# Kernel tuning notes

Hardware: AMD Instinct MI355X
Metric: run time of the kernel (lower is better)

## Reference

```python
import jax, jax.numpy as jnp
import numpy as np

B, N_AIM, N_DET, C = 4, 2048, 2048, 256  # inplanes=256, inter_channels=128


def _lin(x, w, b):
    # torch nn.Linear: y = x @ W^T + b, weight shape [out, in]
    return jnp.einsum('bnc,dc->bnd', x, w) + b


def setup_inputs() -> dict:
    key = jax.random.key(0)
    ks = jax.random.split(key, 16)
    s = 1.0 / np.sqrt(C)
    inp = {
        'detect': jax.random.normal(ks[0], (B, N_DET, C), jnp.float32),
        'aim': jax.random.normal(ks[1], (B, N_AIM, C), jnp.float32),
    }
    names = ['g', 'g2', 'theta', 'phi', 'W', 'Q']
    for i, nm in enumerate(names):
        inp[nm + '_w'] = jax.random.uniform(ks[2 + 2 * i], (C, C), jnp.float32, -s, s)
        inp[nm + '_b'] = jax.random.uniform(ks[3 + 2 * i], (C,), jnp.float32, -s, s)
    return inp


def reference(detect, aim, g_w, g_b, g2_w, g2_b, theta_w, theta_b, phi_w, phi_b, W_w, W_b, Q_w, Q_b):
    b, na, c = aim.shape
    nd = detect.shape[1]
    ic = c // 2  # inter_channels

    # view(B, ic, -1) on a contiguous [B, N, C] tensor -> row-major reshape to [B, ic, 2N]
    d_x = _lin(detect, g_w, g_b).reshape(b, ic, -1).transpose(0, 2, 1)      # (B, 2Nd, ic)
    a_x = _lin(aim, g2_w, g2_b).reshape(b, ic, -1).transpose(0, 2, 1)       # (B, 2Na, ic)
    theta_x = _lin(aim, theta_w, theta_b).reshape(b, ic, -1).transpose(0, 2, 1)  # (B, 2Na, ic)
    phi_x = _lin(detect, phi_w, phi_b).reshape(b, ic, -1)                   # (B, ic, 2Nd)

    f = jnp.matmul(theta_x, phi_x)                 # (B, 2Na, 2Nd)
    f_div_C = f / f.shape[-1]                      # scale by 2*Nd
    fi_div_C = jnp.swapaxes(f, 1, 2) / f.shape[-2] # (B, 2Nd, 2Na), scale by 2*Na

    non_aim = jnp.matmul(f_div_C, d_x)             # (B, 2Na, ic)
    non_aim = non_aim.transpose(0, 2, 1).reshape(b, na, c)
    non_aim = _lin(non_aim, W_w, W_b) + aim

    non_det = jnp.matmul(fi_div_C, a_x)            # (B, 2Nd, ic)
    non_det = non_det.transpose(0, 2, 1).reshape(b, nd, c)
    non_det = _lin(non_det, Q_w, Q_b) + detect

    return (non_det, non_aim)
```

## Files before the change

### kernel.cpp

```cpp
#include <hip/hip_runtime.h>


typedef __attribute__((ext_vector_type(4))) float  f32x4;
typedef __attribute__((ext_vector_type(8))) __bf16 bf16x8;
typedef __attribute__((ext_vector_type(8))) unsigned short u16x8;
typedef __attribute__((ext_vector_type(4))) unsigned short u16x4;

__device__ inline unsigned short f2bf(float f) {
    union { float f; unsigned u; } c; c.f = f;
    unsigned r = c.u + 0x7FFF + ((c.u >> 16) & 1);
    return (unsigned short)(r >> 16);
}
__device__ inline bf16x8 ldfrag(const unsigned short* p) {
    return __builtin_bit_cast(bf16x8, *(const u16x8*)p);
}

__global__ __launch_bounds__(256)
void prep_kernel(const float* __restrict__ g_w, const float* __restrict__ g2_w,
                 const float* __restrict__ th_w, const float* __restrict__ ph_w,
                 const float* __restrict__ W_w, const float* __restrict__ Q_w,
                 const float* __restrict__ aim, const float* __restrict__ detect,
                 unsigned short* __restrict__ dst)
{
    const int z = blockIdx.y;
    const float* src; size_t n4; unsigned short* o;
    if (z == 0)      { src = g_w;    n4 = 16384;  o = dst; }
    else if (z == 1) { src = g2_w;   n4 = 16384;  o = dst + 65536; }
    else if (z == 2) { src = th_w;   n4 = 16384;  o = dst + 2 * 65536; }
    else if (z == 3) { src = ph_w;   n4 = 16384;  o = dst + 3 * 65536; }
    else if (z == 4) { src = W_w;    n4 = 16384;  o = dst + 4 * 65536; }
    else if (z == 5) { src = Q_w;    n4 = 16384;  o = dst + 5 * 65536; }
    else if (z == 6) { src = aim;    n4 = 524288; o = dst + 6 * 65536; }
    else             { src = detect; n4 = 524288; o = dst + 6 * 65536 + 2097152; }
    const size_t stride = (size_t)gridDim.x * 256;
    for (size_t i = blockIdx.x * 256 + threadIdx.x; i < n4; i += stride) {
        float4 v = ((const float4*)src)[i];
        u16x4 p; p[0]=f2bf(v.x); p[1]=f2bf(v.y); p[2]=f2bf(v.z); p[3]=f2bf(v.w);
        ((u16x4*)o)[i] = p;
    }
}

__global__ __launch_bounds__(256)
void lin4_kernel(const unsigned short* __restrict__ Abf, const unsigned short* __restrict__ Dbf,
                 const unsigned short* __restrict__ Wb,
                 const float* __restrict__ b_g, const float* __restrict__ b_g2,
                 const float* __restrict__ b_th, const float* __restrict__ b_ph,
                 unsigned short* __restrict__ T,  unsigned short* __restrict__ Ga,
                 unsigned short* __restrict__ P,  unsigned short* __restrict__ Gd)
{
    const int z = blockIdx.z, set = blockIdx.x;
    const unsigned short* A = z ? Dbf : Abf;
    const int wslot = z ? (set ? 0 : 3) : (set ? 1 : 2);
    const unsigned short* Wm = Wb + (size_t)wslot * 65536;
    const float* Bv = z ? (set ? b_g : b_ph) : (set ? b_g2 : b_th);
    unsigned short* O = z ? (set ? Gd : P) : (set ? Ga : T);
    const int m0 = blockIdx.y * 64;

    __shared__ unsigned short As[64][40];
    __shared__ unsigned short Bs[256][40];

    const int tid = threadIdx.x, lane = tid & 63, w = tid >> 6;
    const int wr = w >> 1, wc = w & 1, q = lane >> 4, ln = lane & 15;

    f32x4 acc[2][8] = {};

    for (int k0 = 0; k0 < 256; k0 += 32) {
        {
            int row = tid >> 2, c8 = tid & 3;
            *(u16x8*)&As[row][c8 * 8] = *(const u16x8*)(A + (size_t)(m0 + row) * 256 + k0 + c8 * 8);
        }
        #pragma unroll
        for (int i = 0; i < 4; ++i) {
            int c = tid + i * 256, row = c >> 2, c8 = c & 3;
            *(u16x8*)&Bs[row][c8 * 8] = *(const u16x8*)(Wm + (size_t)row * 256 + k0 + c8 * 8);
        }
        __syncthreads();
        bf16x8 af[2], bb[8];
        #pragma unroll
        for (int i = 0; i < 2; ++i) af[i] = ldfrag(&As[wr * 32 + i * 16 + ln][q * 8]);
        #pragma unroll
        for (int j = 0; j < 8; ++j) bb[j] = ldfrag(&Bs[wc * 128 + j * 16 + ln][q * 8]);
        #pragma unroll
        for (int i = 0; i < 2; ++i)
            #pragma unroll
            for (int j = 0; j < 8; ++j)
                acc[i][j] = __builtin_amdgcn_mfma_f32_16x16x32_bf16(af[i], bb[j], acc[i][j], 0, 0, 0);
        __syncthreads();
    }

    #pragma unroll
    for (int i = 0; i < 2; ++i)
        #pragma unroll
        for (int j = 0; j < 8; ++j) {
            int n = wc * 128 + j * 16 + ln;
            float bias = Bv[n];
            #pragma unroll
            for (int r = 0; r < 4; ++r) {
                int m = m0 + wr * 32 + i * 16 + q * 4 + r;
                O[(size_t)m * 256 + n] = f2bf(acc[i][j][r] + bias);
            }
        }
}

__global__ __launch_bounds__(256)
void mid_kernel(const unsigned short* __restrict__ Gd, const unsigned short* __restrict__ P,
                const unsigned short* __restrict__ Ga, const unsigned short* __restrict__ T,
                const unsigned short* __restrict__ Wb,
                float* __restrict__ Spart,
                unsigned short* __restrict__ TW, unsigned short* __restrict__ PQ)
{
    __shared__ unsigned short lds[13824];

    const int tid = threadIdx.x, lane = tid & 63, w = tid >> 6;
    const int wr = w >> 1, wc = w & 1, q = lane >> 4, ln = lane & 15;

    if (blockIdx.x < 256) {
        const int bz = blockIdx.x;
        const int which = bz >> 7, rem = bz & 127, batch = rem >> 5;
        const int mhalf = (rem >> 4) & 1, chunk = rem & 15;
        const unsigned short* A = (which ? Ga : Gd) + (size_t)batch * 524288;
        const unsigned short* B = (which ? T  : P ) + (size_t)batch * 524288;
        float* out = Spart + ((size_t)(which * 4 + batch) * 16 + chunk) * 16384;
        const int kbeg = chunk * 256, m0 = mhalf * 64;

        unsigned short (*As)[72] = (unsigned short (*)[72])lds;
        unsigned short (*Bs)[72] = (unsigned short (*)[72])(lds + 64 * 72);

        f32x4 acc[2][4] = {};

        for (int kk = 0; kk < 4; ++kk) {
            const int k0 = kbeg + kk * 64;
            #pragma unroll
            for (int i = 0; i < 2; ++i) {
                int c = tid + i * 256, row = c >> 3, c8 = c & 7;
                *(u16x8*)&As[row][c8 * 8] = *(const u16x8*)(A + (size_t)(m0 + row) * 4096 + k0 + c8 * 8);
            }
            #pragma unroll
            for (int i = 0; i < 4; ++i) {
                int c = tid + i * 256, row = c >> 3, c8 = c & 7;
                *(u16x8*)&Bs[row][c8 * 8] = *(const u16x8*)(B + (size_t)row * 4096 + k0 + c8 * 8);
            }
            __syncthreads();
            #pragma unroll
            for (int ks = 0; ks < 2; ++ks) {
                bf16x8 af[2], bb[4];
                #pragma unroll
                for (int i = 0; i < 2; ++i) af[i] = ldfrag(&As[wr * 32 + i * 16 + ln][ks * 32 + q * 8]);
                #pragma unroll
                for (int j = 0; j < 4; ++j) bb[j] = ldfrag(&Bs[wc * 64 + j * 16 + ln][ks * 32 + q * 8]);
                #pragma unroll
                for (int i = 0; i < 2; ++i)
                    #pragma unroll
                    for (int j = 0; j < 4; ++j)
                        acc[i][j] = __builtin_amdgcn_mfma_f32_16x16x32_bf16(af[i], bb[j], acc[i][j], 0, 0, 0);
            }
            __syncthreads();
        }

        #pragma unroll
        for (int i = 0; i < 2; ++i)
            #pragma unroll
            for (int j = 0; j < 4; ++j)
                #pragma unroll
                for (int r = 0; r < 4; ++r) {
                    int m = m0 + wr * 32 + i * 16 + q * 4 + r, n = wc * 64 + j * 16 + ln;
                    out[m * 128 + n] = acc[i][j][r];
                }
    } else {
        const int t = blockIdx.x - 256;
        const int side = t >> 8, rem = t & 255, mtile = rem >> 1, nhalf = rem & 1;
        const unsigned short* A = side ? P : T;
        const unsigned short* Wm = Wb + (size_t)(4 + side) * 65536;
        unsigned short* O = side ? PQ : TW;
        const int m0 = mtile * 64, n0 = nhalf * 128;

        unsigned short (*As)[40] = (unsigned short (*)[40])lds;
        unsigned short (*Bs)[40] = (unsigned short (*)[40])(lds + 64 * 40);

        f32x4 acc[2][4] = {};

        for (int k0 = 0; k0 < 256; k0 += 32) {
            {
                int row = tid >> 2, c8 = tid & 3;
                *(u16x8*)&As[row][c8 * 8] = *(const u16x8*)(A + (size_t)(m0 + row) * 256 + k0 + c8 * 8);
            }
            #pragma unroll
            for (int i = 0; i < 2; ++i) {
                int c = tid + i * 256, row = c >> 2, c8 = c & 3;
                *(u16x8*)&Bs[row][c8 * 8] = *(const u16x8*)(Wm + (size_t)(n0 + row) * 256 + k0 + c8 * 8);
            }
            __syncthreads();
            bf16x8 af[2], bb[4];
            #pragma unroll
            for (int i = 0; i < 2; ++i) af[i] = ldfrag(&As[wr * 32 + i * 16 + ln][q * 8]);
            #pragma unroll
            for (int j = 0; j < 4; ++j) bb[j] = ldfrag(&Bs[wc * 64 + j * 16 + ln][q * 8]);
            #pragma unroll
            for (int i = 0; i < 2; ++i)
                #pragma unroll
                for (int j = 0; j < 4; ++j)
                    acc[i][j] = __builtin_amdgcn_mfma_f32_16x16x32_bf16(af[i], bb[j], acc[i][j], 0, 0, 0);
            __syncthreads();
        }

        #pragma unroll
        for (int i = 0; i < 2; ++i)
            #pragma unroll
            for (int j = 0; j < 4; ++j) {
                int n = n0 + wc * 64 + j * 16 + ln;
                #pragma unroll
                for (int r = 0; r < 4; ++r) {
                    int m = m0 + wr * 32 + i * 16 + q * 4 + r;
                    O[(size_t)m * 256 + n] = f2bf(acc[i][j][r]);
                }
            }
    }
}

__global__ __launch_bounds__(256)
void sred_kernel(const float* __restrict__ Spart, unsigned short* __restrict__ Sbf)
{
    const int idx = blockIdx.x * 256 + threadIdx.x;
    const int c = idx >> 14, e = idx & 16383;
    float s = 0.f;
    #pragma unroll
    for (int k = 0; k < 16; ++k) s += Spart[((size_t)(c * 16 + k) << 14) + e];
    Sbf[idx] = f2bf(s * (1.0f / 4096.0f));
}

__global__ __launch_bounds__(256)
void combine_kernel(const unsigned short* __restrict__ Sbf,
                    const unsigned short* __restrict__ TW, const unsigned short* __restrict__ PQ,
                    const float* __restrict__ W_b, const float* __restrict__ Q_b,
                    const float* __restrict__ aim, const float* __restrict__ detect,
                    float* __restrict__ out_aim, float* __restrict__ out_det)
{
    const int which = blockIdx.z >> 2, batch = blockIdx.z & 3;
    const int qq = blockIdx.y;
    const int dtile = blockIdx.x >> 1, ihalf = blockIdx.x & 1;
    const int d0 = dtile * 128, i0 = ihalf * 64;
    const unsigned short* Sm = Sbf + (size_t)(which * 4 + batch) * 16384;
    const unsigned short* Bsrc = (which ? PQ : TW) + (size_t)batch * 524288;
    const float* Bv = which ? Q_b : W_b;
    const float* R  = (which ? detect : aim) + (size_t)batch * 524288;
    float* O = (which ? out_det : out_aim) + (size_t)batch * 524288;

    __shared__ unsigned short As[64][72];
    __shared__ unsigned short Bs[128][72];

    const int tid = threadIdx.x, lane = tid & 63, w = tid >> 6;
    const int wr = w >> 1, wc = w & 1, q = lane >> 4, ln = lane & 15;

    f32x4 acc[2][4] = {};

    for (int kk = 0; kk < 2; ++kk) {
        const int k0 = kk * 64;
        #pragma unroll
        for (int i = 0; i < 2; ++i) {
            int c = tid + i * 256, row = c >> 3, c8 = c & 7;
            *(u16x8*)&As[row][c8 * 8] = *(const u16x8*)(Sm + (size_t)(i0 + row) * 128 + k0 + c8 * 8);
        }
        #pragma unroll
        for (int i = 0; i < 4; ++i) {
            int c = tid + i * 256, krow = c >> 4, dc = (c & 15) * 8;
            int gr = 16 * (k0 + krow) + qq;
            u16x8 v = *(const u16x8*)(Bsrc + (size_t)gr * 256 + d0 + dc);
            #pragma unroll
            for (int jj = 0; jj < 8; ++jj) Bs[dc + jj][krow] = v[jj];
        }
        __syncthreads();
        #pragma unroll
        for (int ks = 0; ks < 2; ++ks) {
            bf16x8 af[2], bb[4];
            #pragma unroll
            for (int i = 0; i < 2; ++i) af[i] = ldfrag(&As[wr * 32 + i * 16 + ln][ks * 32 + q * 8]);
            #pragma unroll
            for (int j = 0; j < 4; ++j) bb[j] = ldfrag(&Bs[wc * 64 + j * 16 + ln][ks * 32 + q * 8]);
            #pragma unroll
            for (int i = 0; i < 2; ++i)
                #pragma unroll
                for (int j = 0; j < 4; ++j)
                    acc[i][j] = __builtin_amdgcn_mfma_f32_16x16x32_bf16(af[i], bb[j], acc[i][j], 0, 0, 0);
        }
        __syncthreads();
    }

    #pragma unroll
    for (int i = 0; i < 2; ++i)
        #pragma unroll
        for (int j = 0; j < 4; ++j) {
            int d = d0 + wc * 64 + j * 16 + ln;
            float bias = Bv[d];
            #pragma unroll
            for (int r = 0; r < 4; ++r) {
                int iS = i0 + wr * 32 + i * 16 + q * 4 + r;
                size_t off = (size_t)(16 * iS + qq) * 256 + d;
                O[off] = acc[i][j][r] + bias + R[off];
            }
        }
}

extern "C" void kernel_launch(void* const* d_in, const int* in_sizes, int n_in,
                              void* d_out, int out_size, void* d_ws, size_t ws_size,
                              hipStream_t stream)
{
    const float* detect = (const float*)d_in[0];
    const float* aim    = (const float*)d_in[1];
    const float* g_w  = (const float*)d_in[2];  const float* g_b  = (const float*)d_in[3];
    const float* g2_w = (const float*)d_in[4];  const float* g2_b = (const float*)d_in[5];
    const float* th_w = (const float*)d_in[6];  const float* th_b = (const float*)d_in[7];
    const float* ph_w = (const float*)d_in[8];  const float* ph_b = (const float*)d_in[9];
    const float* W_w  = (const float*)d_in[10]; const float* W_b  = (const float*)d_in[11];
    const float* Q_w  = (const float*)d_in[12]; const float* Q_b  = (const float*)d_in[13];

    const size_t TOT = 8192L * 256;

    unsigned short* ws16 = (unsigned short*)d_ws;
    unsigned short* Wbf = ws16;
    unsigned short* Abf = Wbf + 6 * 65536;
    unsigned short* Dbf = Abf + TOT;
    unsigned short* T   = Dbf + TOT;
    unsigned short* P   = T  + TOT;
    unsigned short* Gd  = P  + TOT;
    unsigned short* Ga  = Gd + TOT;
    unsigned short* TW  = Ga + TOT;
    unsigned short* PQ  = TW + TOT;
    unsigned short* Sbf = PQ + TOT;
    float* Spart = (float*)(Sbf + 131072);

    float* out_det = (float*)d_out;
    float* out_aim = out_det + TOT;

    prep_kernel<<<dim3(256, 8), 256, 0, stream>>>(
        g_w, g2_w, th_w, ph_w, W_w, Q_w, aim, detect, Wbf);
    lin4_kernel<<<dim3(2, 128, 2), 256, 0, stream>>>(
        Abf, Dbf, Wbf, g_b, g2_b, th_b, ph_b, T, Ga, P, Gd);
    mid_kernel<<<dim3(768), 256, 0, stream>>>(Gd, P, Ga, T, Wbf, Spart, TW, PQ);
    sred_kernel<<<dim3(512), 256, 0, stream>>>(Spart, Sbf);
    combine_kernel<<<dim3(4, 16, 8), 256, 0, stream>>>(
        Sbf, TW, PQ, W_b, Q_b, aim, detect, out_aim, out_det);
}
```

Before: 143.2 us.

## Fuse all five stages into one persistent kernel with grid barriers

Replaces the five separate launches (prep, linear projections, mid GEMMs, reduction, combine) with a single 512-block persistent kernel. The stages are separated by atomic-counter grid barriers that are reset by a memset each call. The f-matrix partial GEMM is re-tiled to 64x64 outputs so it fits into 512 blocks, and the W/Q projection is placed in the same barrier phase. The aim is to remove launch gaps and tail effects between kernels. In exchange it relies on all 512 blocks being co-resident, adds barrier spin overhead, and sets occupancy via launch_bounds(256,2).

```diff
diff --git a/kernel.cpp b/kernel.cpp
--- a/kernel.cpp
+++ b/kernel.cpp
@@ -15,130 +15,251 @@
     return __builtin_bit_cast(bf16x8, *(const u16x8*)p);
 }
 
-__global__ __launch_bounds__(256)
-void prep_kernel(const float* __restrict__ g_w, const float* __restrict__ g2_w,
-                 const float* __restrict__ th_w, const float* __restrict__ ph_w,
-                 const float* __restrict__ W_w, const float* __restrict__ Q_w,
-                 const float* __restrict__ aim, const float* __restrict__ detect,
-                 unsigned short* __restrict__ dst)
-{
-    const int z = blockIdx.y;
-    const float* src; size_t n4; unsigned short* o;
-    if (z == 0)      { src = g_w;    n4 = 16384;  o = dst; }
-    else if (z == 1) { src = g2_w;   n4 = 16384;  o = dst + 65536; }
-    else if (z == 2) { src = th_w;   n4 = 16384;  o = dst + 2 * 65536; }
-    else if (z == 3) { src = ph_w;   n4 = 16384;  o = dst + 3 * 65536; }
-    else if (z == 4) { src = W_w;    n4 = 16384;  o = dst + 4 * 65536; }
-    else if (z == 5) { src = Q_w;    n4 = 16384;  o = dst + 5 * 65536; }
-    else if (z == 6) { src = aim;    n4 = 524288; o = dst + 6 * 65536; }
-    else             { src = detect; n4 = 524288; o = dst + 6 * 65536 + 2097152; }
-    const size_t stride = (size_t)gridDim.x * 256;
-    for (size_t i = blockIdx.x * 256 + threadIdx.x; i < n4; i += stride) {
-        float4 v = ((const float4*)src)[i];
-        u16x4 p; p[0]=f2bf(v.x); p[1]=f2bf(v.y); p[2]=f2bf(v.z); p[3]=f2bf(v.w);
-        ((u16x4*)o)[i] = p;
-    }
-}
-
-__global__ __launch_bounds__(256)
-void lin4_kernel(const unsigned short* __restrict__ Abf, const unsigned short* __restrict__ Dbf,
-                 const unsigned short* __restrict__ Wb,
-                 const float* __restrict__ b_g, const float* __restrict__ b_g2,
-                 const float* __restrict__ b_th, const float* __restrict__ b_ph,
-                 unsigned short* __restrict__ T,  unsigned short* __restrict__ Ga,
-                 unsigned short* __restrict__ P,  unsigned short* __restrict__ Gd)
-{
-    const int z = blockIdx.z, set = blockIdx.x;
-    const unsigned short* A = z ? Dbf : Abf;
-    const int wslot = z ? (set ? 0 : 3) : (set ? 1 : 2);
-    const unsigned short* Wm = Wb + (size_t)wslot * 65536;
-    const float* Bv = z ? (set ? b_g : b_ph) : (set ? b_g2 : b_th);
-    unsigned short* O = z ? (set ? Gd : P) : (set ? Ga : T);
-    const int m0 = blockIdx.y * 64;
-
-    __shared__ unsigned short As[64][40];
-    __shared__ unsigned short Bs[256][40];
-
-    const int tid = threadIdx.x, lane = tid & 63, w = tid >> 6;
-    const int wr = w >> 1, wc = w & 1, q = lane >> 4, ln = lane & 15;
-
-    f32x4 acc[2][8] = {};
-
-    for (int k0 = 0; k0 < 256; k0 += 32) {
-        {
-            int row = tid >> 2, c8 = tid & 3;
-            *(u16x8*)&As[row][c8 * 8] = *(const u16x8*)(A + (size_t)(m0 + row) * 256 + k0 + c8 * 8);
-        }
-        #pragma unroll
-        for (int i = 0; i < 4; ++i) {
-            int c = tid + i * 256, row = c >> 2, c8 = c & 3;
-            *(u16x8*)&Bs[row][c8 * 8] = *(const u16x8*)(Wm + (size_t)row * 256 + k0 + c8 * 8);
-        }
-        __syncthreads();
-        bf16x8 af[2], bb[8];
-        #pragma unroll
-        for (int i = 0; i < 2; ++i) af[i] = ldfrag(&As[wr * 32 + i * 16 + ln][q * 8]);
-        #pragma unroll
-        for (int j = 0; j < 8; ++j) bb[j] = ldfrag(&Bs[wc * 128 + j * 16 + ln][q * 8]);
-        #pragma unroll
-        for (int i = 0; i < 2; ++i)
-            #pragma unroll
-            for (int j = 0; j < 8; ++j)
-                acc[i][j] = __builtin_amdgcn_mfma_f32_16x16x32_bf16(af[i], bb[j], acc[i][j], 0, 0, 0);
-        __syncthreads();
-    }
-
-    #pragma unroll
-    for (int i = 0; i < 2; ++i)
-        #pragma unroll
-        for (int j = 0; j < 8; ++j) {
-            int n = wc * 128 + j * 16 + ln;
-            float bias = Bv[n];
-            #pragma unroll
-            for (int r = 0; r < 4; ++r) {
-                int m = m0 + wr * 32 + i * 16 + q * 4 + r;
-                O[(size_t)m * 256 + n] = f2bf(acc[i][j][r] + bias);
-            }
-        }
-}
-
-__global__ __launch_bounds__(256)
-void mid_kernel(const unsigned short* __restrict__ Gd, const unsigned short* __restrict__ P,
-                const unsigned short* __restrict__ Ga, const unsigned short* __restrict__ T,
-                const unsigned short* __restrict__ Wb,
-                float* __restrict__ Spart,
-                unsigned short* __restrict__ TW, unsigned short* __restrict__ PQ)
+#define NBLK 512u
+
+__device__ inline void gridbar(unsigned* bar, int slot) {
+    __syncthreads();
+    if (threadIdx.x == 0) {
+        __threadfence();
+        __hip_atomic_fetch_add(bar + slot, 1u, __ATOMIC_RELAXED, __HIP_MEMORY_SCOPE_AGENT);
+        while (__hip_atomic_load(bar + slot, __ATOMIC_RELAXED, __HIP_MEMORY_SCOPE_AGENT) < NBLK)
+            __builtin_amdgcn_s_sleep(8);
+        __threadfence();
+    }
+    __syncthreads();
+}
+
+struct MegaArgs {
+    const float *detect, *aim;
+    const float *g_w, *g2_w, *th_w, *ph_w, *W_w, *Q_w;
+    const float *b_g, *b_g2, *b_th, *b_ph, *b_W, *b_Q;
+    unsigned short *Wbf, *Abf, *Dbf, *T, *P, *Gd, *Ga, *TW, *PQ, *Sbf;
+    float *Spart, *out_aim, *out_det;
+    unsigned *bar;
+};
+
+__global__ __launch_bounds__(256, 2)
+void mega_kernel(MegaArgs a)
 {
     __shared__ unsigned short lds[13824];
 
-    const int tid = threadIdx.x, lane = tid & 63, w = tid >> 6;
+    const int bid = blockIdx.x, tid = threadIdx.x;
+    const int lane = tid & 63, w = tid >> 6;
     const int wr = w >> 1, wc = w & 1, q = lane >> 4, ln = lane & 15;
 
-    if (blockIdx.x < 256) {
-        const int bz = blockIdx.x;
-        const int which = bz >> 7, rem = bz & 127, batch = rem >> 5;
-        const int mhalf = (rem >> 4) & 1, chunk = rem & 15;
-        const unsigned short* A = (which ? Ga : Gd) + (size_t)batch * 524288;
-        const unsigned short* B = (which ? T  : P ) + (size_t)batch * 524288;
-        float* out = Spart + ((size_t)(which * 4 + batch) * 16 + chunk) * 16384;
-        const int kbeg = chunk * 256, m0 = mhalf * 64;
+    if (bid < 44) {
+        for (int i = bid * 256 + tid; i < 98304; i += 44 * 256) {
+            int wsel = i >> 14, off = i & 16383;
+            const float* src = wsel == 0 ? a.g_w : wsel == 1 ? a.g2_w : wsel == 2 ? a.th_w :
+                               wsel == 3 ? a.ph_w : wsel == 4 ? a.W_w : a.Q_w;
+            float4 v = ((const float4*)src)[off];
+            u16x4 p; p[0]=f2bf(v.x); p[1]=f2bf(v.y); p[2]=f2bf(v.z); p[3]=f2bf(v.w);
+            ((u16x4*)(a.Wbf + (size_t)wsel * 65536))[off] = p;
+        }
+    } else {
+        const int r = bid - 44;
+        const float* src = r < 234 ? a.aim : a.detect;
+        unsigned short* o = r < 234 ? a.Abf : a.Dbf;
+        const int rb = r < 234 ? r : r - 234;
+        for (int i = rb * 256 + tid; i < 524288; i += 234 * 256) {
+            float4 v = ((const float4*)src)[i];
+            u16x4 p; p[0]=f2bf(v.x); p[1]=f2bf(v.y); p[2]=f2bf(v.z); p[3]=f2bf(v.w);
+            ((u16x4*)o)[i] = p;
+        }
+    }
+    gridbar(a.bar, 0);
+
+    {
+        const int z = bid >> 8, rem = bid & 255, set = rem & 1, mtile = rem >> 1;
+        const unsigned short* Ap = z ? a.Dbf : a.Abf;
+        const int wslot = z ? (set ? 0 : 3) : (set ? 1 : 2);
+        const unsigned short* Wm = a.Wbf + (size_t)wslot * 65536;
+        const float* Bv = z ? (set ? a.b_g : a.b_ph) : (set ? a.b_g2 : a.b_th);
+        unsigned short* O = z ? (set ? a.Gd : a.P) : (set ? a.Ga : a.T);
+        const int m0 = mtile * 64;
+
+        unsigned short (*As)[40] = (unsigned short (*)[40])lds;
+        unsigned short (*Bs)[40] = (unsigned short (*)[40])(lds + 64 * 40);
+
+        f32x4 acc[2][8] = {};
+
+        for (int k0 = 0; k0 < 256; k0 += 32) {
+            {
+                int row = tid >> 2, c8 = tid & 3;
+                *(u16x8*)&As[row][c8 * 8] = *(const u16x8*)(Ap + (size_t)(m0 + row) * 256 + k0 + c8 * 8);
+            }
+            #pragma unroll
+            for (int i = 0; i < 4; ++i) {
+                int c = tid + i * 256, row = c >> 2, c8 = c & 3;
+                *(u16x8*)&Bs[row][c8 * 8] = *(const u16x8*)(Wm + (size_t)row * 256 + k0 + c8 * 8);
+            }
+            __syncthreads();
+            bf16x8 af[2], bb[8];
+            #pragma unroll
+            for (int i = 0; i < 2; ++i) af[i] = ldfrag(&As[wr * 32 + i * 16 + ln][q * 8]);
+            #pragma unroll
+            for (int j = 0; j < 8; ++j) bb[j] = ldfrag(&Bs[wc * 128 + j * 16 + ln][q * 8]);
+            #pragma unroll
+            for (int i = 0; i < 2; ++i)
+                #pragma unroll
+                for (int j = 0; j < 8; ++j)
+                    acc[i][j] = __builtin_amdgcn_mfma_f32_16x16x32_bf16(af[i], bb[j], acc[i][j], 0, 0, 0);
+            __syncthreads();
+        }
+
+        #pragma unroll
+        for (int i = 0; i < 2; ++i)
+            #pragma unroll
+            for (int j = 0; j < 8; ++j) {
+                int n = wc * 128 + j * 16 + ln;
+                float bias = Bv[n];
+                #pragma unroll
+                for (int r = 0; r < 4; ++r) {
+                    int m = m0 + wr * 32 + i * 16 + q * 4 + r;
+                    O[(size_t)m * 256 + n] = f2bf(acc[i][j][r] + bias);
+                }
+            }
+    }
+    gridbar(a.bar, 1);
+
+    {
+        const int side = bid >> 8, rem = bid & 255, mtile = rem >> 1, nhalf = rem & 1;
+        const unsigned short* Ap = side ? a.P : a.T;
+        const unsigned short* Wm = a.Wbf + (size_t)(4 + side) * 65536;
+        unsigned short* O = side ? a.PQ : a.TW;
+        const int m0 = mtile * 64, n0 = nhalf * 128;
+
+        unsigned short (*As)[40] = (unsigned short (*)[40])lds;
+        unsigned short (*Bs)[40] = (unsigned short (*)[40])(lds + 64 * 40);
+
+        f32x4 acc[2][4] = {};
+
+        for (int k0 = 0; k0 < 256; k0 += 32) {
+            {
+                int row = tid >> 2, c8 = tid & 3;
+                *(u16x8*)&As[row][c8 * 8] = *(const u16x8*)(Ap + (size_t)(m0 + row) * 256 + k0 + c8 * 8);
+            }
+            #pragma unroll
+            for (int i = 0; i < 2; ++i) {
+                int c = tid + i * 256, row = c >> 2, c8 = c & 3;
+                *(u16x8*)&Bs[row][c8 * 8] = *(const u16x8*)(Wm + (size_t)(n0 + row) * 256 + k0 + c8 * 8);
+            }
+            __syncthreads();
+            bf16x8 af[2], bb[4];
+            #pragma unroll
+            for (int i = 0; i < 2; ++i) af[i] = ldfrag(&As[wr * 32 + i * 16 + ln][q * 8]);
+            #pragma unroll
+            for (int j = 0; j < 4; ++j) bb[j] = ldfrag(&Bs[wc * 64 + j * 16 + ln][q * 8]);
+            #pragma unroll
+            for (int i = 0; i < 2; ++i)
+                #pragma unroll
+                for (int j = 0; j < 4; ++j)
+                    acc[i][j] = __builtin_amdgcn_mfma_f32_16x16x32_bf16(af[i], bb[j], acc[i][j], 0, 0, 0);
+            __syncthreads();
+        }
+
+        #pragma unroll
+        for (int i = 0; i < 2; ++i)
+            #pragma unroll
+            for (int j = 0; j < 4; ++j) {
+                int n = n0 + wc * 64 + j * 16 + ln;
+                #pragma unroll
+                for (int r = 0; r < 4; ++r) {
+                    int m = m0 + wr * 32 + i * 16 + q * 4 + r;
+                    O[(size_t)m * 256 + n] = f2bf(acc[i][j][r]);
+                }
+            }
+    }
+
+    {
+        const int which = bid >> 8, rem = bid & 255, batch = rem >> 6, rem2 = rem & 63;
+        const int mt = rem2 >> 5, nt = (rem2 >> 4) & 1, chunk = rem2 & 15;
+        const unsigned short* Ap = (which ? a.Ga : a.Gd) + (size_t)batch * 524288;
+        const unsigned short* Bp = (which ? a.T  : a.P ) + (size_t)batch * 524288;
+        float* out = a.Spart + ((size_t)(which * 4 + batch) * 16 + chunk) * 16384;
+        const int kbeg = chunk * 256, m0 = mt * 64, n0 = nt * 64;
 
         unsigned short (*As)[72] = (unsigned short (*)[72])lds;
         unsigned short (*Bs)[72] = (unsigned short (*)[72])(lds + 64 * 72);
 
-        f32x4 acc[2][4] = {};
+        f32x4 acc[2][2] = {};
 
         for (int kk = 0; kk < 4; ++kk) {
             const int k0 = kbeg + kk * 64;
             #pragma unroll
             for (int i = 0; i < 2; ++i) {
                 int c = tid + i * 256, row = c >> 3, c8 = c & 7;
-                *(u16x8*)&As[row][c8 * 8] = *(const u16x8*)(A + (size_t)(m0 + row) * 4096 + k0 + c8 * 8);
+                *(u16x8*)&As[row][c8 * 8] = *(const u16x8*)(Ap + (size_t)(m0 + row) * 4096 + k0 + c8 * 8);
+                *(u16x8*)&Bs[row][c8 * 8] = *(const u16x8*)(Bp + (size_t)(n0 + row) * 4096 + k0 + c8 * 8);
+            }
+            __syncthreads();
+            #pragma unroll
+            for (int ks = 0; ks < 2; ++ks) {
+                bf16x8 af[2], bb[2];
+                #pragma unroll
+                for (int i = 0; i < 2; ++i) af[i] = ldfrag(&As[wr * 32 + i * 16 + ln][ks * 32 + q * 8]);
+                #pragma unroll
+                for (int j = 0; j < 2; ++j) bb[j] = ldfrag(&Bs[wc * 32 + j * 16 + ln][ks * 32 + q * 8]);
+                #pragma unroll
+                for (int i = 0; i < 2; ++i)
+                    #pragma unroll
+                    for (int j = 0; j < 2; ++j)
+                        acc[i][j] = __builtin_amdgcn_mfma_f32_16x16x32_bf16(af[i], bb[j], acc[i][j], 0, 0, 0);
+            }
+            __syncthreads();
+        }
+
+        #pragma unroll
+        for (int i = 0; i < 2; ++i)
+            #pragma unroll
+            for (int j = 0; j < 2; ++j)
+                #pragma unroll
+                for (int r = 0; r < 4; ++r) {
+                    int m = m0 + wr * 32 + i * 16 + q * 4 + r, n = n0 + wc * 32 + j * 16 + ln;
+                    out[m * 128 + n] = acc[i][j][r];
+                }
+    }
+    gridbar(a.bar, 2);
+
+    {
+        const int idx = bid * 256 + tid;
+        const int c = idx >> 14, e = idx & 16383;
+        float s = 0.f;
+        #pragma unroll
+        for (int k = 0; k < 16; ++k) s += a.Spart[((size_t)(c * 16 + k) << 14) + e];
+        a.Sbf[idx] = f2bf(s * (1.0f / 4096.0f));
+    }
+    gridbar(a.bar, 3);
+
+    {
+        const int which = bid >> 8, batch = (bid >> 6) & 3, qq = (bid >> 2) & 15;
+        const int dtile = (bid >> 1) & 1, ihalf = bid & 1;
+        const int d0 = dtile * 128, i0 = ihalf * 64;
+        const unsigned short* Sm = a.Sbf + (size_t)(which * 4 + batch) * 16384;
+        const unsigned short* Bsrc = (which ? a.PQ : a.TW) + (size_t)batch * 524288;
+        const float* Bv = which ? a.b_Q : a.b_W;
+        const float* R  = (which ? a.detect : a.aim) + (size_t)batch * 524288;
+        float* O = (which ? a.out_det : a.out_aim) + (size_t)batch * 524288;
+
+        unsigned short (*As)[72] = (unsigned short (*)[72])lds;
+        unsigned short (*Bs)[72] = (unsigned short (*)[72])(lds + 64 * 72);
+
+        f32x4 acc[2][4] = {};
+
+        for (int kk = 0; kk < 2; ++kk) {
+            const int k0 = kk * 64;
+            #pragma unroll
+            for (int i = 0; i < 2; ++i) {
+                int c = tid + i * 256, row = c >> 3, c8 = c & 7;
+                *(u16x8*)&As[row][c8 * 8] = *(const u16x8*)(Sm + (size_t)(i0 + row) * 128 + k0 + c8 * 8);
             }
             #pragma unroll
             for (int i = 0; i < 4; ++i) {
-                int c = tid + i * 256, row = c >> 3, c8 = c & 7;
-                *(u16x8*)&Bs[row][c8 * 8] = *(const u16x8*)(B + (size_t)row * 4096 + k0 + c8 * 8);
+                int c = tid + i * 256, krow = c >> 4, dc = (c & 15) * 8;
+                int gr = 16 * (k0 + krow) + qq;
+                u16x8 v = *(const u16x8*)(Bsrc + (size_t)gr * 256 + d0 + dc);
+                #pragma unroll
+                for (int jj = 0; jj < 8; ++jj) Bs[dc + jj][krow] = v[jj];
             }
             __syncthreads();
             #pragma unroll
@@ -160,159 +281,23 @@
         #pragma unroll
         for (int i = 0; i < 2; ++i)
             #pragma unroll
-            for (int j = 0; j < 4; ++j)
+            for (int j = 0; j < 4; ++j) {
+                int d = d0 + wc * 64 + j * 16 + ln;
+                float bias = Bv[d];
                 #pragma unroll
                 for (int r = 0; r < 4; ++r) {
-                    int m = m0 + wr * 32 + i * 16 + q * 4 + r, n = wc * 64 + j * 16 + ln;
-                    out[m * 128 + n] = acc[i][j][r];
+                    int iS = i0 + wr * 32 + i * 16 + q * 4 + r;
+                    size_t off = (size_t)(16 * iS + qq) * 256 + d;
+                    O[off] = acc[i][j][r] + bias + R[off];
                 }
-    } else {
-        const int t = blockIdx.x - 256;
-        const int side = t >> 8, rem = t & 255, mtile = rem >> 1, nhalf = rem & 1;
-        const unsigned short* A = side ? P : T;
-        const unsigned short* Wm = Wb + (size_t)(4 + side) * 65536;
-        unsigned short* O = side ? PQ : TW;
-        const int m0 = mtile * 64, n0 = nhalf * 128;
-
-        unsigned short (*As)[40] = (unsigned short (*)[40])lds;
-        unsigned short (*Bs)[40] = (unsigned short (*)[40])(lds + 64 * 40);
-
-        f32x4 acc[2][4] = {};
-
-        for (int k0 = 0; k0 < 256; k0 += 32) {
-            {
-                int row = tid >> 2, c8 = tid & 3;
-                *(u16x8*)&As[row][c8 * 8] = *(const u16x8*)(A + (size_t)(m0 + row) * 256 + k0 + c8 * 8);
-            }
-            #pragma unroll
-            for (int i = 0; i < 2; ++i) {
-                int c = tid + i * 256, row = c >> 2, c8 = c & 3;
-                *(u16x8*)&Bs[row][c8 * 8] = *(const u16x8*)(Wm + (size_t)(n0 + row) * 256 + k0 + c8 * 8);
-            }
-            __syncthreads();
-            bf16x8 af[2], bb[4];
-            #pragma unroll
-            for (int i = 0; i < 2; ++i) af[i] = ldfrag(&As[wr * 32 + i * 16 + ln][q * 8]);
-            #pragma unroll
-            for (int j = 0; j < 4; ++j) bb[j] = ldfrag(&Bs[wc * 64 + j * 16 + ln][q * 8]);
-            #pragma unroll
-            for (int i = 0; i < 2; ++i)
-                #pragma unroll
-                for (int j = 0; j < 4; ++j)
-                    acc[i][j] = __builtin_amdgcn_mfma_f32_16x16x32_bf16(af[i], bb[j], acc[i][j], 0, 0, 0);
-            __syncthreads();
-        }
-
-        #pragma unroll
-        for (int i = 0; i < 2; ++i)
-            #pragma unroll
-            for (int j = 0; j < 4; ++j) {
-                int n = n0 + wc * 64 + j * 16 + ln;
-                #pragma unroll
-                for (int r = 0; r < 4; ++r) {
-                    int m = m0 + wr * 32 + i * 16 + q * 4 + r;
-                    O[(size_t)m * 256 + n] = f2bf(acc[i][j][r]);
-                }
-            }
-    }
-}
-
-__global__ __launch_bounds__(256)
-void sred_kernel(const float* __restrict__ Spart, unsigned short* __restrict__ Sbf)
-{
-    const int idx = blockIdx.x * 256 + threadIdx.x;
-    const int c = idx >> 14, e = idx & 16383;
-    float s = 0.f;
-    #pragma unroll
-    for (int k = 0; k < 16; ++k) s += Spart[((size_t)(c * 16 + k) << 14) + e];
-    Sbf[idx] = f2bf(s * (1.0f / 4096.0f));
-}
-
-__global__ __launch_bounds__(256)
-void combine_kernel(const unsigned short* __restrict__ Sbf,
-                    const unsigned short* __restrict__ TW, const unsigned short* __restrict__ PQ,
-                    const float* __restrict__ W_b, const float* __restrict__ Q_b,
-                    const float* __restrict__ aim, const float* __restrict__ detect,
-                    float* __restrict__ out_aim, float* __restrict__ out_det)
-{
-    const int which = blockIdx.z >> 2, batch = blockIdx.z & 3;
-    const int qq = blockIdx.y;
-    const int dtile = blockIdx.x >> 1, ihalf = blockIdx.x & 1;
-    const int d0 = dtile * 128, i0 = ihalf * 64;
-    const unsigned short* Sm = Sbf + (size_t)(which * 4 + batch) * 16384;
-    const unsigned short* Bsrc = (which ? PQ : TW) + (size_t)batch * 524288;
-    const float* Bv = which ? Q_b : W_b;
-    const float* R  = (which ? detect : aim) + (size_t)batch * 524288;
-    float* O = (which ? out_det : out_aim) + (size_t)batch * 524288;
-
-    __shared__ unsigned short As[64][72];
-    __shared__ unsigned short Bs[128][72];
-
-    const int tid = threadIdx.x, lane = tid & 63, w = tid >> 6;
-    const int wr = w >> 1, wc = w & 1, q = lane >> 4, ln = lane & 15;
-
-    f32x4 acc[2][4] = {};
-
-    for (int kk = 0; kk < 2; ++kk) {
-        const int k0 = kk * 64;
-        #pragma unroll
-        for (int i = 0; i < 2; ++i) {
-            int c = tid + i * 256, row = c >> 3, c8 = c & 7;
-            *(u16x8*)&As[row][c8 * 8] = *(const u16x8*)(Sm + (size_t)(i0 + row) * 128 + k0 + c8 * 8);
-        }
-        #pragma unroll
-        for (int i = 0; i < 4; ++i) {
-            int c = tid + i * 256, krow = c >> 4, dc = (c & 15) * 8;
-            int gr = 16 * (k0 + krow) + qq;
-            u16x8 v = *(const u16x8*)(Bsrc + (size_t)gr * 256 + d0 + dc);
-            #pragma unroll
-            for (int jj = 0; jj < 8; ++jj) Bs[dc + jj][krow] = v[jj];
-        }
-        __syncthreads();
-        #pragma unroll
-        for (int ks = 0; ks < 2; ++ks) {
-            bf16x8 af[2], bb[4];
-            #pragma unroll
-            for (int i = 0; i < 2; ++i) af[i] = ldfrag(&As[wr * 32 + i * 16 + ln][ks * 32 + q * 8]);
-            #pragma unroll
-            for (int j = 0; j < 4; ++j) bb[j] = ldfrag(&Bs[wc * 64 + j * 16 + ln][ks * 32 + q * 8]);
-            #pragma unroll
-            for (int i = 0; i < 2; ++i)
-                #pragma unroll
-                for (int j = 0; j < 4; ++j)
-                    acc[i][j] = __builtin_amdgcn_mfma_f32_16x16x32_bf16(af[i], bb[j], acc[i][j], 0, 0, 0);
-        }
-        __syncthreads();
-    }
-
-    #pragma unroll
-    for (int i = 0; i < 2; ++i)
-        #pragma unroll
-        for (int j = 0; j < 4; ++j) {
-            int d = d0 + wc * 64 + j * 16 + ln;
-            float bias = Bv[d];
-            #pragma unroll
-            for (int r = 0; r < 4; ++r) {
-                int iS = i0 + wr * 32 + i * 16 + q * 4 + r;
-                size_t off = (size_t)(16 * iS + qq) * 256 + d;
-                O[off] = acc[i][j][r] + bias + R[off];
-            }
-        }
+            }
+    }
 }
 
 extern "C" void kernel_launch(void* const* d_in, const int* in_sizes, int n_in,
                               void* d_out, int out_size, void* d_ws, size_t ws_size,
                               hipStream_t stream)
 {
-    const float* detect = (const float*)d_in[0];
-    const float* aim    = (const float*)d_in[1];
-    const float* g_w  = (const float*)d_in[2];  const float* g_b  = (const float*)d_in[3];
-    const float* g2_w = (const float*)d_in[4];  const float* g2_b = (const float*)d_in[5];
-    const float* th_w = (const float*)d_in[6];  const float* th_b = (const float*)d_in[7];
-    const float* ph_w = (const float*)d_in[8];  const float* ph_b = (const float*)d_in[9];
-    const float* W_w  = (const float*)d_in[10]; const float* W_b  = (const float*)d_in[11];
-    const float* Q_w  = (const float*)d_in[12]; const float* Q_b  = (const float*)d_in[13];
-
     const size_t TOT = 8192L * 256;
 
     unsigned short* ws16 = (unsigned short*)d_ws;
@@ -327,16 +312,25 @@
     unsigned short* PQ  = TW + TOT;
     unsigned short* Sbf = PQ + TOT;
     float* Spart = (float*)(Sbf + 131072);
+    unsigned* bar = (unsigned*)(Spart + (size_t)2 * 4 * 16 * 16384);
 
     float* out_det = (float*)d_out;
     float* out_aim = out_det + TOT;
 
-    prep_kernel<<<dim3(256, 8), 256, 0, stream>>>(
-        g_w, g2_w, th_w, ph_w, W_w, Q_w, aim, detect, Wbf);
-    lin4_kernel<<<dim3(2, 128, 2), 256, 0, stream>>>(
-        Abf, Dbf, Wbf, g_b, g2_b, th_b, ph_b, T, Ga, P, Gd);
-    mid_kernel<<<dim3(768), 256, 0, stream>>>(Gd, P, Ga, T, Wbf, Spart, TW, PQ);
-    sred_kernel<<<dim3(512), 256, 0, stream>>>(Spart, Sbf);
-    combine_kernel<<<dim3(4, 16, 8), 256, 0, stream>>>(
-        Sbf, TW, PQ, W_b, Q_b, aim, detect, out_aim, out_det);
-}
+    MegaArgs h;
+    h.detect = (const float*)d_in[0];
+    h.aim    = (const float*)d_in[1];
+    h.g_w  = (const float*)d_in[2];  h.b_g  = (const float*)d_in[3];
+    h.g2_w = (const float*)d_in[4];  h.b_g2 = (const float*)d_in[5];
+    h.th_w = (const float*)d_in[6];  h.b_th = (const float*)d_in[7];
+    h.ph_w = (const float*)d_in[8];  h.b_ph = (const float*)d_in[9];
+    h.W_w  = (const float*)d_in[10]; h.b_W  = (const float*)d_in[11];
+    h.Q_w  = (const float*)d_in[12]; h.b_Q  = (const float*)d_in[13];
+    h.Wbf = Wbf; h.Abf = Abf; h.Dbf = Dbf; h.T = T; h.P = P;
+    h.Gd = Gd; h.Ga = Ga; h.TW = TW; h.PQ = PQ; h.Sbf = Sbf;
+    h.Spart = Spart; h.out_aim = out_aim; h.out_det = out_det;
+    h.bar = bar;
+
+    hipMemsetAsync(bar, 0, 64, stream);
+    mega_kernel<<<dim3(512), dim3(256), 0, stream>>>(h);
+}
```

New measurement: 333.1 us. 2.33x slower.
